# Performance work log

Measured on AMD Instinct MI355X. Metric: run time of the kernel, lower is better.

Reference implementation:

```python
import jax, jax.numpy as jnp
import numpy as np


def _nn_sq_dists(query, ref):
    # query: [B, N, 3], ref: [B, M, 3]
    # squared distance via ||q||^2 + ||r||^2 - 2 q.r, min over ref points
    q2 = jnp.sum(query * query, axis=-1)            # [B, N]
    r2 = jnp.sum(ref * ref, axis=-1)                # [B, M]
    cross = jnp.einsum('bnc,bmc->bnm', query, ref)  # [B, N, M]
    d = q2[:, :, None] + r2[:, None, :] - 2.0 * cross
    d = jnp.maximum(d, 0.0)  # clamp numerical negatives (true distances >= 0)
    return jnp.min(d, axis=-1)                      # [B, N] 1-NN squared dists


def setup_inputs() -> dict:
    key = jax.random.key(0)
    k1, k2 = jax.random.split(key)
    B, C, N = 4, 3, 8192
    pc2 = jax.random.normal(k1, (B, C, N), dtype=jnp.float32)
    pc1_warped = jax.random.normal(k2, (B, C, N), dtype=jnp.float32)
    return {"pc2": pc2, "pc1_warped": pc1_warped}


def reference(pc2, pc1_warped):
    # pos1 = target['pc2'], pos2 = output['pc1_warped'], both [B, 3, N]
    pos1 = jnp.transpose(pc2, (0, 2, 1))         # [B, N, 3]
    pos2 = jnp.transpose(pc1_warped, (0, 2, 1))  # [B, N, 3]
    # pointutils.knn(1, pos1, pos2): for each pos1 point, nearest in pos2.
    nn_d = _nn_sq_dists(pos1, pos2)              # [B, N]
    per_batch = jnp.sum(nn_d, axis=1)            # sum over dim 1
    loss = per_batch.mean() + per_batch.mean()
    return loss
```

## Files before the change

kernel.cpp:

```cpp
#include <hip/hip_runtime.h>


#define NPTS    8192
#define NB      4
#define TOTQ    (NB * NPTS)
#define BQ      256
#define QT      8
#define QPB     (BQ * QT)
#define MC      256
#define MP      (MC / 2)
#define MCHUNKS (NPTS / MC)

typedef float v2f __attribute__((ext_vector_type(2)));

#if __has_builtin(__builtin_elementwise_fma)
#define VFMA(a, b, c) __builtin_elementwise_fma((a), (b), (c))
#else
#define VFMA(a, b, c) ((a) * (b) + (c))
#endif

__global__ __launch_bounds__(BQ) void chamfer_partial(
    const float* __restrict__ pc2,
    const float* __restrict__ pc1w,
    float* __restrict__ partial,
    float* __restrict__ out)
{
    __shared__ v2f lds[MP * 4];
    const int tid = threadIdx.x;
    const int b  = blockIdx.z;
    const int m0 = blockIdx.y * MC;
    const int q0 = blockIdx.x * QPB;

    if (blockIdx.x == 0 && blockIdx.y == 0 && blockIdx.z == 0 && tid == 0)
        out[0] = 0.0f;

    const float* refb = pc1w + b * 3 * NPTS;
    {
        int i = tid;
        float rx = refb[m0 + i];
        float ry = refb[NPTS + m0 + i];
        float rz = refb[2 * NPTS + m0 + i];
        float h  = -0.5f * (rx * rx + ry * ry + rz * rz);
        float* lf = (float*)lds;
        int base = (i >> 1) * 8 + (i & 1);
        lf[base + 0] = rx;
        lf[base + 2] = ry;
        lf[base + 4] = rz;
        lf[base + 6] = h;
    }
    __syncthreads();

    const float* qb = pc2 + b * 3 * NPTS;
    v2f qx2[QT], qy2[QT], qz2[QT];
    float smax[QT];
#pragma unroll
    for (int g4 = 0; g4 < 2; ++g4) {
        int off = q0 + g4 * (BQ * 4);
        float4 fx = ((const float4*)(qb + off))[tid];
        float4 fy = ((const float4*)(qb + NPTS + off))[tid];
        float4 fz = ((const float4*)(qb + 2 * NPTS + off))[tid];
        int j = g4 * 4;
        qx2[j+0] = (v2f){fx.x, fx.x}; qx2[j+1] = (v2f){fx.y, fx.y};
        qx2[j+2] = (v2f){fx.z, fx.z}; qx2[j+3] = (v2f){fx.w, fx.w};
        qy2[j+0] = (v2f){fy.x, fy.x}; qy2[j+1] = (v2f){fy.y, fy.y};
        qy2[j+2] = (v2f){fy.z, fy.z}; qy2[j+3] = (v2f){fy.w, fy.w};
        qz2[j+0] = (v2f){fz.x, fz.x}; qz2[j+1] = (v2f){fz.y, fz.y};
        qz2[j+2] = (v2f){fz.z, fz.z}; qz2[j+3] = (v2f){fz.w, fz.w};
    }
#pragma unroll
    for (int j = 0; j < QT; ++j) smax[j] = -1e30f;

#pragma unroll 2
    for (int p = 0; p < MP; ++p) {
        v2f rx = lds[p * 4 + 0];
        v2f ry = lds[p * 4 + 1];
        v2f rz = lds[p * 4 + 2];
        v2f rh = lds[p * 4 + 3];
#pragma unroll
        for (int j = 0; j < QT; ++j) {
            v2f s = VFMA(qx2[j], rx, rh);
            s = VFMA(qy2[j], ry, s);
            s = VFMA(qz2[j], rz, s);
            smax[j] = fmaxf(smax[j], fmaxf(s[0], s[1]));
        }
    }

    float* pbase = partial + blockIdx.y * TOTQ + b * NPTS;
#pragma unroll
    for (int g4 = 0; g4 < 2; ++g4) {
        int off = q0 + g4 * (BQ * 4);
        int j = g4 * 4;
        float4 o = make_float4(smax[j], smax[j+1], smax[j+2], smax[j+3]);
        ((float4*)(pbase + off))[tid] = o;
    }
}

__global__ __launch_bounds__(512) void chamfer_reduce(
    const float* __restrict__ pc2,
    const float* __restrict__ partial,
    float* __restrict__ out)
{
    const int g = blockIdx.x * 512 + threadIdx.x;
    float smax = -1e30f;
#pragma unroll
    for (int c = 0; c < MCHUNKS; ++c)
        smax = fmaxf(smax, partial[c * TOTQ + g]);

    const int b = g >> 13;
    const int n = g & (NPTS - 1);
    const float* qb = pc2 + b * 3 * NPTS;
    float qx = qb[n], qy = qb[NPTS + n], qz = qb[2 * NPTS + n];
    float q2 = qx * qx + qy * qy + qz * qz;
    float d = fmaxf(q2 - 2.0f * smax, 0.0f);

#pragma unroll
    for (int off = 32; off > 0; off >>= 1)
        d += __shfl_down(d, off, 64);

    __shared__ float wsum[8];
    const int lane = threadIdx.x & 63;
    const int wid  = threadIdx.x >> 6;
    if (lane == 0) wsum[wid] = d;
    __syncthreads();
    if (threadIdx.x == 0) {
        float s = 0.0f;
#pragma unroll
        for (int w = 0; w < 8; ++w) s += wsum[w];
        atomicAdd(out, s * (2.0f / NB));
    }
}

extern "C" void kernel_launch(void* const* d_in, const int* in_sizes, int n_in,
                              void* d_out, int out_size, void* d_ws, size_t ws_size,
                              hipStream_t stream) {
    const float* pc2  = (const float*)d_in[0];
    const float* pc1w = (const float*)d_in[1];
    float* out = (float*)d_out;
    float* partial = (float*)d_ws;

    dim3 g1(NPTS / QPB, MCHUNKS, NB);
    chamfer_partial<<<g1, BQ, 0, stream>>>(pc2, pc1w, partial, out);
    chamfer_reduce<<<TOTQ / 512, 512, 0, stream>>>(pc2, partial, out);
}
```

Baseline: 80.13 us.

## Drop packed v2f FMA for scalar FMAs, halve ref chunk size, float4 LDS layout

Replaces the packed two-wide float FMA (v_pk_fma_f32) inner loop with scalar fmaf on reference points stored as float4 {x,y,z,h} in shared memory. The reference chunk per block is halved to 128, which doubles the number of blocks and partial-max chunks, and the unroll factors change. The aim is likely more parallelism and simpler LDS reads. The cost is losing packed-math throughput, roughly doubling FMA instruction count, plus doubled partial-buffer traffic in the reduce kernel.

```diff
diff --git a/kernel.cpp b/kernel.cpp
--- a/kernel.cpp
+++ b/kernel.cpp
@@ -7,17 +7,9 @@
 #define BQ      256
 #define QT      8
 #define QPB     (BQ * QT)
-#define MC      256
+#define MC      128
 #define MP      (MC / 2)
 #define MCHUNKS (NPTS / MC)
-
-typedef float v2f __attribute__((ext_vector_type(2)));
-
-#if __has_builtin(__builtin_elementwise_fma)
-#define VFMA(a, b, c) __builtin_elementwise_fma((a), (b), (c))
-#else
-#define VFMA(a, b, c) ((a) * (b) + (c))
-#endif
 
 __global__ __launch_bounds__(BQ) void chamfer_partial(
     const float* __restrict__ pc2,
@@ -25,7 +17,7 @@
     float* __restrict__ partial,
     float* __restrict__ out)
 {
-    __shared__ v2f lds[MP * 4];
+    __shared__ float4 lds[MC];
     const int tid = threadIdx.x;
     const int b  = blockIdx.z;
     const int m0 = blockIdx.y * MC;
@@ -35,24 +27,18 @@
         out[0] = 0.0f;
 
     const float* refb = pc1w + b * 3 * NPTS;
-    {
+    if (tid < MC) {
         int i = tid;
         float rx = refb[m0 + i];
         float ry = refb[NPTS + m0 + i];
         float rz = refb[2 * NPTS + m0 + i];
         float h  = -0.5f * (rx * rx + ry * ry + rz * rz);
-        float* lf = (float*)lds;
-        int base = (i >> 1) * 8 + (i & 1);
-        lf[base + 0] = rx;
-        lf[base + 2] = ry;
-        lf[base + 4] = rz;
-        lf[base + 6] = h;
+        lds[i] = make_float4(rx, ry, rz, h);
     }
     __syncthreads();
 
     const float* qb = pc2 + b * 3 * NPTS;
-    v2f qx2[QT], qy2[QT], qz2[QT];
-    float smax[QT];
+    float qx[QT], qy[QT], qz[QT], smax[QT];
 #pragma unroll
     for (int g4 = 0; g4 < 2; ++g4) {
         int off = q0 + g4 * (BQ * 4);
@@ -60,28 +46,26 @@
         float4 fy = ((const float4*)(qb + NPTS + off))[tid];
         float4 fz = ((const float4*)(qb + 2 * NPTS + off))[tid];
         int j = g4 * 4;
-        qx2[j+0] = (v2f){fx.x, fx.x}; qx2[j+1] = (v2f){fx.y, fx.y};
-        qx2[j+2] = (v2f){fx.z, fx.z}; qx2[j+3] = (v2f){fx.w, fx.w};
-        qy2[j+0] = (v2f){fy.x, fy.x}; qy2[j+1] = (v2f){fy.y, fy.y};
-        qy2[j+2] = (v2f){fy.z, fy.z}; qy2[j+3] = (v2f){fy.w, fy.w};
-        qz2[j+0] = (v2f){fz.x, fz.x}; qz2[j+1] = (v2f){fz.y, fz.y};
-        qz2[j+2] = (v2f){fz.z, fz.z}; qz2[j+3] = (v2f){fz.w, fz.w};
+        qx[j+0] = fx.x; qx[j+1] = fx.y; qx[j+2] = fx.z; qx[j+3] = fx.w;
+        qy[j+0] = fy.x; qy[j+1] = fy.y; qy[j+2] = fy.z; qy[j+3] = fy.w;
+        qz[j+0] = fz.x; qz[j+1] = fz.y; qz[j+2] = fz.z; qz[j+3] = fz.w;
     }
 #pragma unroll
     for (int j = 0; j < QT; ++j) smax[j] = -1e30f;
 
-#pragma unroll 2
+#pragma unroll 4
     for (int p = 0; p < MP; ++p) {
-        v2f rx = lds[p * 4 + 0];
-        v2f ry = lds[p * 4 + 1];
-        v2f rz = lds[p * 4 + 2];
-        v2f rh = lds[p * 4 + 3];
+        float4 r0 = lds[2 * p + 0];
+        float4 r1 = lds[2 * p + 1];
 #pragma unroll
         for (int j = 0; j < QT; ++j) {
-            v2f s = VFMA(qx2[j], rx, rh);
-            s = VFMA(qy2[j], ry, s);
-            s = VFMA(qz2[j], rz, s);
-            smax[j] = fmaxf(smax[j], fmaxf(s[0], s[1]));
+            float s0 = fmaf(qx[j], r0.x, r0.w);
+            s0 = fmaf(qy[j], r0.y, s0);
+            s0 = fmaf(qz[j], r0.z, s0);
+            float s1 = fmaf(qx[j], r1.x, r1.w);
+            s1 = fmaf(qy[j], r1.y, s1);
+            s1 = fmaf(qz[j], r1.z, s1);
+            smax[j] = fmaxf(smax[j], fmaxf(s0, s1));
         }
     }
 
@@ -102,7 +86,7 @@
 {
     const int g = blockIdx.x * 512 + threadIdx.x;
     float smax = -1e30f;
-#pragma unroll
+#pragma unroll 8
     for (int c = 0; c < MCHUNKS; ++c)
         smax = fmaxf(smax, partial[c * TOTQ + g]);
 
```

New measurement: 88.59 us. 10.6% more time.
